# Optimization experiments

Hardware: AMD Instinct MI355X
Metric: run time of the kernel (lower is better)

## Reference

```python
import jax, jax.numpy as jnp
import numpy as np

DIM = 256
NUM_HEADS = 4
HEAD_DIM = DIM // NUM_HEADS
SCALE = HEAD_DIM ** -0.5


def setup_inputs() -> dict:
    key = jax.random.key(0)
    ks = jax.random.split(key, 11)
    B, Nq, Nkv = 4, 2048, 2048
    inp = {
        "query_feat": jax.random.normal(ks[0], (B, Nq, DIM), dtype=jnp.float32),
        "key_value_feat": jax.random.normal(ks[1], (B, Nkv, DIM), dtype=jnp.float32),
        "reliability_kv": jax.random.uniform(ks[2], (B, Nkv), dtype=jnp.float32),
        "Wq": jax.random.normal(ks[3], (DIM, DIM), dtype=jnp.float32) * (DIM ** -0.5),
        "bq": jnp.zeros((DIM,), jnp.float32),
        "Wk": jax.random.normal(ks[4], (DIM, DIM), dtype=jnp.float32) * (DIM ** -0.5),
        "bk": jnp.zeros((DIM,), jnp.float32),
        "Wv": jax.random.normal(ks[5], (DIM, DIM), dtype=jnp.float32) * (DIM ** -0.5),
        "bv": jnp.zeros((DIM,), jnp.float32),
        "Wo": jax.random.normal(ks[6], (DIM, DIM), dtype=jnp.float32) * (DIM ** -0.5),
        "bo": jnp.zeros((DIM,), jnp.float32),
    }
    return inp


def _heads(x):
    B, N, C = x.shape
    return x.reshape(B, N, NUM_HEADS, HEAD_DIM).transpose(0, 2, 1, 3)  # [B,H,N,hd]


def reference(query_feat, key_value_feat, reliability_kv, Wq, bq, Wk, bk, Wv, bv, Wo, bo):
    B, Nq, _ = query_feat.shape
    q = _heads(query_feat @ Wq + bq)          # [B,H,Nq,hd]
    k = _heads(key_value_feat @ Wk + bk)      # [B,H,Nkv,hd]
    v = _heads(key_value_feat @ Wv + bv)
    # gate K/V by reliability (broadcast over heads and head_dim)
    rk = reliability_kv[:, None, :, None]     # [B,1,Nkv,1]
    k = k * rk
    v = v * rk
    attn = jnp.einsum("bhqd,bhkd->bhqk", q, k) * SCALE
    log_r = jnp.log(jnp.clip(reliability_kv, 1e-6))[:, None, None, :]  # [B,1,1,Nkv]
    attn = jax.nn.softmax(attn + log_r, axis=-1)  # [B,H,Nq,Nkv]
    out = jnp.einsum("bhqk,bhkd->bhqd", attn, v)
    out = out.transpose(0, 2, 1, 3).reshape(B, Nq, DIM)
    out = out @ Wo + bo
    attn_mean = attn.mean(axis=1)  # [B,Nq,Nkv]
    return out, attn_mean
```

## Files before the change

kernel.cpp:

```cpp
#include <hip/hip_runtime.h>


typedef __attribute__((ext_vector_type(8))) _Float16 half8;
typedef __attribute__((ext_vector_type(4))) _Float16 half4;
typedef __attribute__((ext_vector_type(2))) __fp16 fp16x2;
typedef __attribute__((ext_vector_type(4))) float f32x4;

#define MFMAH32(A, B, C) __builtin_amdgcn_mfma_f32_16x16x32_f16((A), (B), (C), 0, 0, 0)
#define MFMAH16(A, B, C) __builtin_amdgcn_mfma_f32_16x16x16f16((A), (B), (C), 0, 0, 0)

__device__ __forceinline__ unsigned short f2h(float f) {
    union { _Float16 h; unsigned short u; } c; c.h = (_Float16)f; return c.u;
}
__device__ __forceinline__ float h2f(unsigned short u) {
    union { unsigned short u; _Float16 h; } c; c.u = u; return (float)c.h;
}
__device__ __forceinline__ half8 ldh8(const unsigned short* p) {
    return *reinterpret_cast<const half8*>(p);
}
__device__ __forceinline__ half4 ldh4(const unsigned short* p) {
    return *reinterpret_cast<const half4*>(p);
}
__device__ __forceinline__ half4 pk4(float a, float b, float c, float d) {
    union { fp16x2 h2[2]; half4 h4; } u;
    u.h2[0] = __builtin_amdgcn_cvt_pkrtz(a, b);
    u.h2[1] = __builtin_amdgcn_cvt_pkrtz(c, d);
    return u.h4;
}
__device__ __forceinline__ unsigned int pku(float a, float b) {
    union { fp16x2 h2; unsigned int u; } c;
    c.h2 = __builtin_amdgcn_cvt_pkrtz(a, b);
    return c.u;
}
__device__ __forceinline__ void gld16(const unsigned short* g, unsigned short* l) {
    __builtin_amdgcn_global_load_lds(
        (const __attribute__((address_space(1))) unsigned int*)g,
        (__attribute__((address_space(3))) unsigned int*)l, 16, 0, 0);
}

__global__ void wsplit_kernel(const float* __restrict__ Wq, const float* __restrict__ Wk,
                              const float* __restrict__ Wv, const float* __restrict__ Wo,
                              unsigned short* __restrict__ WT) {
    int e = blockIdx.x * 256 + threadIdx.x;
    int m = e >> 16;
    int idx = e & 65535;
    int k = idx >> 8, n = idx & 255;
    const float* W = (m == 0) ? Wq : (m == 1) ? Wk : (m == 2) ? Wv : Wo;
    WT[m * 65536 + n * 256 + k] = f2h(W[idx]);
}

#define STAGE_W(dst_, src_, kt_) do {                                               \
    _Pragma("unroll")                                                               \
    for (int j_ = 0; j_ < 4; ++j_) {                                                \
        int s_ = w * 4 + j_;                                                        \
        int rowl_ = 8 * s_ + (l >> 3);                                              \
        int so_ = rowl_ * 256 + (kt_) * 64 + (((l & 7) ^ (rowl_ & 7)) << 3);        \
        gld16(&(src_)[so_], &(dst_)[s_ * 512]);                                     \
    }                                                                               \
} while (0)

#define GEMM_TILE(buf_, kt_) do {                                                   \
    _Pragma("unroll")                                                               \
    for (int ksl_ = 0; ksl_ < 2; ++ksl_) {                                          \
        _Pragma("unroll")                                                           \
        for (int n_ = 0; n_ < 16; ++n_) {                                           \
            int r_ = n_ * 16 + l15;                                                 \
            int idx_ = r_ * 64 + ((((ksl_)*4 + lg) ^ (r_ & 7)) << 3);               \
            half8 b_ = ldh8(&(buf_)[idx_]);                                         \
            acc[n_] = MFMAH32(ah[(kt_) * 2 + ksl_], b_, acc[n_]);                   \
        }                                                                           \
    }                                                                               \
} while (0)

__global__ __launch_bounds__(512, 1) void proj3_kernel(
    const float* __restrict__ query, const float* __restrict__ kv,
    const float* __restrict__ rel, const unsigned short* __restrict__ WT,
    const float* __restrict__ bq, const float* __restrict__ bk, const float* __restrict__ bv,
    unsigned short* __restrict__ Qh, unsigned short* __restrict__ Kh,
    unsigned short* __restrict__ Vtmp) {
    const int job = blockIdx.y;
    const float* X = (job == 0) ? query : kv;
    const unsigned short* wg = WT + job * 65536;
    const float* bias = (job == 0) ? bq : (job == 1) ? bk : bv;
    const float* rs = (job == 0) ? nullptr : rel;
    unsigned short* oh = (job == 0) ? Qh : (job == 1) ? Kh : Vtmp;

    __shared__ __align__(16) unsigned short wlds[2][256 * 64];

    const int w = threadIdx.x >> 6, l = threadIdx.x & 63;
    const int l15 = l & 15, lg = l >> 4;
    const int arow = blockIdx.x * 128 + w * 16 + l15;

    half8 ah[8];
#pragma unroll
    for (int ks = 0; ks < 8; ++ks) {
        const float* p = &X[arow * 256 + ks * 32 + lg * 8];
        float4 f0 = *reinterpret_cast<const float4*>(p);
        float4 f1 = *reinterpret_cast<const float4*>(p + 4);
        half8 t;
        t[0] = (_Float16)f0.x; t[1] = (_Float16)f0.y; t[2] = (_Float16)f0.z; t[3] = (_Float16)f0.w;
        t[4] = (_Float16)f1.x; t[5] = (_Float16)f1.y; t[6] = (_Float16)f1.z; t[7] = (_Float16)f1.w;
        ah[ks] = t;
    }
    f32x4 acc[16];
#pragma unroll
    for (int n = 0; n < 16; ++n) acc[n] = (f32x4){0.f, 0.f, 0.f, 0.f};

    STAGE_W(wlds[0], wg, 0);
    __syncthreads();
#pragma unroll
    for (int kt = 0; kt < 4; ++kt) {
        const int cur = kt & 1, nx = cur ^ 1;
        if (kt < 3) STAGE_W(wlds[nx], wg, kt + 1);
        GEMM_TILE(wlds[cur], kt);
        __syncthreads();
    }

    const int orow0 = blockIdx.x * 128 + w * 16 + lg * 4;
    float rsv[4];
#pragma unroll
    for (int r = 0; r < 4; ++r) rsv[r] = rs ? rs[orow0 + r] : 1.0f;
#pragma unroll
    for (int n = 0; n < 16; ++n) {
        const int col = n * 16 + l15;
        const float bn = bias[col];
#pragma unroll
        for (int r = 0; r < 4; ++r)
            oh[(orow0 + r) * 256 + col] = f2h((acc[n][r] + bn) * rsv[r]);
    }
}

__global__ void transpose_v_kernel(const unsigned short* __restrict__ Vtmp,
                                   unsigned short* __restrict__ Vt) {
    __shared__ unsigned short tile[16][264];
    const int st = blockIdx.x, b = blockIdx.y;
    const int t = threadIdx.x;
#pragma unroll
    for (int it = 0; it < 4; ++it) {
        int idx = it * 256 + t;
        int kr = idx >> 6;
        int d4 = (idx & 63) * 4;
        ushort4 v = *reinterpret_cast<const ushort4*>(
            &Vtmp[(size_t)(b * 2048 + st * 16 + kr) * 256 + d4]);
        tile[kr][d4 + 0] = v.x; tile[kr][d4 + 1] = v.y;
        tile[kr][d4 + 2] = v.z; tile[kr][d4 + 3] = v.w;
    }
    __syncthreads();
    {
        const int d = t;
        unsigned int u[8];
#pragma unroll
        for (int k2 = 0; k2 < 8; ++k2)
            u[k2] = (unsigned int)tile[k2 * 2][d] | ((unsigned int)tile[k2 * 2 + 1][d] << 16);
        uint4* dst = reinterpret_cast<uint4*>(&Vt[((size_t)(b * 128 + st) * 256 + d) * 16]);
        dst[0] = (uint4){u[0], u[1], u[2], u[3]};
        dst[1] = (uint4){u[4], u[5], u[6], u[7]};
    }
}

__global__ __launch_bounds__(512, 4) void attn_pass1(
    const unsigned short* __restrict__ Qh, const unsigned short* __restrict__ Kh,
    const unsigned short* __restrict__ Vt, const float* __restrict__ rel,
    float* __restrict__ po_a, float* __restrict__ po_b, float* __restrict__ ps) {
    const int bid = blockIdx.x;
    const int sw = (bid & 7) * 64 + (bid >> 3);
    const int b = sw >> 7;
    const int rem = sw & 127;
    const int kh = rem & 1;
    const int q0 = (rem >> 1) * 32;
    const int tid = threadIdx.x;
    const int w = tid >> 6, h = w & 3, ks = w >> 2;
    const int l = tid & 63, l15 = l & 15, lg = l >> 4;
    const float C2 = 0.18033688011112042f;

    __shared__ __align__(16) unsigned short ldsK[8][2][1024];
    __shared__ __align__(16) unsigned short ldsV[8][2][1024];
    __shared__ float rel_lr[2048];
    __shared__ float ssum_sh[2][4][2][16];

    {
        float4 v = reinterpret_cast<const float4*>(&rel[b * 2048])[tid];
        float* d = &rel_lr[tid * 4];
        d[0] = log2f(fmaxf(v.x, 1e-6f)); d[1] = log2f(fmaxf(v.y, 1e-6f));
        d[2] = log2f(fmaxf(v.z, 1e-6f)); d[3] = log2f(fmaxf(v.w, 1e-6f));
    }

    half8 qf00, qf01, qf10, qf11;
    {
        const int o0 = (b * 2048 + q0 + l15) * 256 + h * 64 + lg * 8;
        const int o1 = o0 + 16 * 256;
        qf00 = ldh8(&Qh[o0]); qf01 = ldh8(&Qh[o0 + 32]);
        qf10 = ldh8(&Qh[o1]); qf11 = ldh8(&Qh[o1 + 32]);
    }
    __syncthreads();

    const int st0 = kh * 64 + ks * 32;

#define STG(buf_, i_) do {                                                          \
    const unsigned short* kbp_ = Kh + (size_t)(b * 2048 + (st0 + (i_)) * 16) * 256  \
                                 + h * 64;                                          \
    _Pragma("unroll")                                                               \
    for (int j_ = 0; j_ < 2; ++j_) {                                                \
        int r_ = j_ * 8 + (l >> 3);                                                 \
        gld16(kbp_ + r_ * 256 + (((l & 7) ^ ((l >> 3) & 7)) << 3),                  \
              &ldsK[w][buf_][j_ * 512]);                                            \
    }                                                                               \
    const unsigned short* vbp_ = Vt + (size_t)((b * 128 + st0 + (i_)) * 256         \
                                 + h * 64) * 16;                                    \
    _Pragma("unroll")                                                               \
    for (int j_ = 0; j_ < 2; ++j_) {                                                \
        int d_ = j_ * 32 + (l >> 1);                                                \
        gld16(vbp_ + d_ * 16 + (((l & 1) ^ ((l >> 1) & 1)) << 3),                   \
              &ldsV[w][buf_][j_ * 512]);                                            \
    }                                                                               \
} while (0)

    float ssum0 = 0.f, ssum1 = 0.f;
    f32x4 o0acc[4], o1acc[4];
#pragma unroll
    for (int dc = 0; dc < 4; ++dc) {
        o0acc[dc] = (f32x4){0.f, 0.f, 0.f, 0.f};
        o1acc[dc] = (f32x4){0.f, 0.f, 0.f, 0.f};
    }

    STG(0, 0);
    for (int i = 0; i < 32; ++i) {
        const int cur = i & 1, nx = cur ^ 1;
        if (i < 31) {
            STG(nx, i + 1);
            asm volatile("s_waitcnt vmcnt(4)" ::: "memory");
        } else {
            asm volatile("s_waitcnt vmcnt(0)" ::: "memory");
        }
        __builtin_amdgcn_sched_barrier(0);
        half8 kf0 = ldh8(&ldsK[w][cur][l15 * 64 + ((lg ^ (l15 & 7)) << 3)]);
        half8 kf1 = ldh8(&ldsK[w][cur][l15 * 64 + (((4 + lg) ^ (l15 & 7)) << 3)]);
        f32x4 a0 = (f32x4){0.f, 0.f, 0.f, 0.f}, a1 = a0;
        a0 = MFMAH32(kf0, qf00, a0); a0 = MFMAH32(kf1, qf01, a0);
        a1 = MFMAH32(kf0, qf10, a1); a1 = MFMAH32(kf1, qf11, a1);
        float4 lr4 = *reinterpret_cast<const float4*>(&rel_lr[(st0 + i) * 16 + lg * 4]);
        float p00 = exp2f(__builtin_fmaf(a0[0], C2, lr4.x));
        float p01 = exp2f(__builtin_fmaf(a0[1], C2, lr4.y));
        float p02 = exp2f(__builtin_fmaf(a0[2], C2, lr4.z));
        float p03 = exp2f(__builtin_fmaf(a0[3], C2, lr4.w));
        float p10 = exp2f(__builtin_fmaf(a1[0], C2, lr4.x));
        float p11 = exp2f(__builtin_fmaf(a1[1], C2, lr4.y));
        float p12 = exp2f(__builtin_fmaf(a1[2], C2, lr4.z));
        float p13 = exp2f(__builtin_fmaf(a1[3], C2, lr4.w));
        ssum0 += (p00 + p01) + (p02 + p03);
        ssum1 += (p10 + p11) + (p12 + p13);
        half4 pa0 = pk4(p00, p01, p02, p03);
        half4 pa1 = pk4(p10, p11, p12, p13);
#pragma unroll
        for (int dc = 0; dc < 4; ++dc) {
            const int d = dc * 16 + l15;
            half4 vf = ldh4(&ldsV[w][cur][d * 16 + ((((lg >> 1) ^ (d & 1))) << 3) + (lg & 1) * 4]);
            o0acc[dc] = MFMAH16(pa0, vf, o0acc[dc]);
            o1acc[dc] = MFMAH16(pa1, vf, o1acc[dc]);
        }
    }
#undef STG

    float v0 = ssum0, v1 = ssum1;
    v0 += __shfl_xor(v0, 16); v0 += __shfl_xor(v0, 32);
    v1 += __shfl_xor(v1, 16); v1 += __shfl_xor(v1, 32);

    __syncthreads();
    if (l < 16) { ssum_sh[ks][h][0][l] = v0; ssum_sh[ks][h][1][l] = v1; }
    float* obuf = (float*)&ldsK[0][0][0];
    if (ks == 1) {
#pragma unroll
        for (int dc = 0; dc < 4; ++dc)
#pragma unroll
            for (int r = 0; r < 4; ++r) {
                const int d = h * 64 + dc * 16 + l15;
                obuf[(lg * 4 + r) * 256 + d] = o0acc[dc][r];
                obuf[(16 + lg * 4 + r) * 256 + d] = o1acc[dc][r];
            }
    }
    __syncthreads();
    if (ks == 0) {
        const int chunk = b * 2 + kh;
        float* po = (chunk < 2) ? (po_a + (size_t)chunk * 524288)
                                : (po_b + (size_t)(chunk - 2) * 524288);
#pragma unroll
        for (int dc = 0; dc < 4; ++dc)
#pragma unroll
            for (int r = 0; r < 4; ++r) {
                const int d = h * 64 + dc * 16 + l15;
                const int qa = lg * 4 + r, qb = 16 + lg * 4 + r;
                po[(size_t)(q0 + qa) * 256 + d] = o0acc[dc][r] + obuf[qa * 256 + d];
                po[(size_t)(q0 + qb) * 256 + d] = o1acc[dc][r] + obuf[qb * 256 + d];
            }
        if (l < 16) {
            ps[(chunk * 4 + h) * 2048 + q0 + l] =
                ssum_sh[0][h][0][l] + ssum_sh[1][h][0][l];
            ps[(chunk * 4 + h) * 2048 + q0 + 16 + l] =
                ssum_sh[0][h][1][l] + ssum_sh[1][h][1][l];
        }
    }
}

__global__ __launch_bounds__(256) void combine_kernel(
    const float* __restrict__ po_a, const float* __restrict__ po_b,
    const float* __restrict__ ps, unsigned short* __restrict__ AO,
    float* __restrict__ sinv_ws) {
    const int t = blockIdx.x * 256 + threadIdx.x;
    const int d4 = t & 63;
    const int bq = t >> 6;
    const int q = bq & 2047;
    const int b = bq >> 11;
    const int d0 = d4 * 4, h = d0 >> 6;
    const int c0 = b * 2, c1 = b * 2 + 1;
    const float* p0 = (c0 < 2) ? po_a + (size_t)c0 * 524288 : po_b + (size_t)(c0 - 2) * 524288;
    const float* p1 = (c1 < 2) ? po_a + (size_t)c1 * 524288 : po_b + (size_t)(c1 - 2) * 524288;
    float4 x = *reinterpret_cast<const float4*>(&p0[(size_t)q * 256 + d0]);
    float4 y = *reinterpret_cast<const float4*>(&p1[(size_t)q * 256 + d0]);
    float s = ps[(c0 * 4 + h) * 2048 + q] + ps[(c1 * 4 + h) * 2048 + q];
    float si = 1.0f / s;
    ushort4 o;
    o.x = f2h((x.x + y.x) * si); o.y = f2h((x.y + y.y) * si);
    o.z = f2h((x.z + y.z) * si); o.w = f2h((x.w + y.w) * si);
    *reinterpret_cast<ushort4*>(&AO[((size_t)(b * 2048 + q)) * 256 + d0]) = o;
    if (d4 == (h << 4)) sinv_ws[(b * 4 + h) * 2048 + q] = si;
}

__global__ __launch_bounds__(256, 2) void attn_mean_kernel(
    const unsigned short* __restrict__ Qh, const unsigned short* __restrict__ Kh,
    const float* __restrict__ rel, const float* __restrict__ sinv_ws,
    float* __restrict__ attn_mean) {
    const int kslice = blockIdx.x >> 8;
    const int inner = blockIdx.x & 255;
    const int sw = (inner & 7) * 32 + (inner >> 3);
    const int b = sw >> 6;
    const int q0 = (sw & 63) * 32;
    const int tid = threadIdx.x;
    const int w = tid >> 6;
    const int h = w;
    const int l = tid & 63, l15 = l & 15, lg = l >> 4;
    const int kb = b * 2048;
    const float C2 = 0.18033688011112042f;

    __shared__ __align__(16) unsigned short ldsK[2][8192];
    __shared__ __align__(16) unsigned short pbf2[2][4][2][640];
    __shared__ float rel_lr[2048];

#define STAGE_KM(dst_, kt_) do {                                                    \
    _Pragma("unroll")                                                               \
    for (int j_ = 0; j_ < 4; ++j_) {                                                \
        int s_ = w * 4 + j_;                                                        \
        int r_ = 2 * s_ + (l >> 5);                                                 \
        size_t so_ = (size_t)(kb + (kt_) * 32 + r_) * 256 +                         \
                     (((l & 31) ^ (r_ & 7)) << 3);                                  \
        gld16(&Kh[so_], &(dst_)[s_ * 512]);                                         \
    }                                                                               \
} while (0)

    {
        float4 v0 = reinterpret_cast<const float4*>(&rel[b * 2048])[tid * 2];
        float4 v1 = reinterpret_cast<const float4*>(&rel[b * 2048])[tid * 2 + 1];
        float* d = &rel_lr[tid * 8];
        d[0] = log2f(fmaxf(v0.x, 1e-6f)); d[1] = log2f(fmaxf(v0.y, 1e-6f));
        d[2] = log2f(fmaxf(v0.z, 1e-6f)); d[3] = log2f(fmaxf(v0.w, 1e-6f));
        d[4] = log2f(fmaxf(v1.x, 1e-6f)); d[5] = log2f(fmaxf(v1.y, 1e-6f));
        d[6] = log2f(fmaxf(v1.z, 1e-6f)); d[7] = log2f(fmaxf(v1.w, 1e-6f));
    }

    half8 qf00, qf01, qf10, qf11;
    {
        const int o0 = (b * 2048 + q0 + l15) * 256 + h * 64 + lg * 8;
        const int o1 = o0 + 16 * 256;
        qf00 = ldh8(&Qh[o0]); qf01 = ldh8(&Qh[o0 + 32]);
        qf10 = ldh8(&Qh[o1]); qf11 = ldh8(&Qh[o1 + 32]);
    }
    const float lsi0 = log2f(sinv_ws[(b * 4 + h) * 2048 + q0 + l15]) - 2.0f;
    const float lsi1 = log2f(sinv_ws[(b * 4 + h) * 2048 + q0 + 16 + l15]) - 2.0f;
    __syncthreads();

    const int kt0 = kslice * 8;
    STAGE_KM(ldsK[0], kt0);
    for (int ki = 0; ki < 8; ++ki) {
        const int kt = kt0 + ki;
        const int cur = ki & 1, nx = cur ^ 1;
        if (ki < 7) {
            STAGE_KM(ldsK[nx], kt + 1);
            asm volatile("s_waitcnt vmcnt(4)" ::: "memory");
        } else {
            asm volatile("s_waitcnt vmcnt(0)" ::: "memory");
        }
        asm volatile("s_barrier" ::: "memory");
        __builtin_amdgcn_sched_barrier(0);
#pragma unroll
        for (int kc = 0; kc < 2; ++kc) {
            const int r = kc * 16 + l15;
            const int rx = r & 7;
            half8 kf0 = ldh8(&ldsK[cur][r * 256 + (((h * 8 + lg) ^ rx) << 3)]);
            half8 kf1 = ldh8(&ldsK[cur][r * 256 + (((h * 8 + 4 + lg) ^ rx) << 3)]);
            f32x4 a0 = (f32x4){0.f, 0.f, 0.f, 0.f}, a1 = a0;
            a0 = MFMAH32(kf0, qf00, a0); a0 = MFMAH32(kf1, qf01, a0);
            a1 = MFMAH32(kf0, qf10, a1); a1 = MFMAH32(kf1, qf11, a1);
            float4 lr4 = *reinterpret_cast<const float4*>(
                &rel_lr[kt * 32 + kc * 16 + lg * 4]);
            float q00 = exp2f(__builtin_fmaf(a0[0], C2, lsi0) + lr4.x);
            float q01 = exp2f(__builtin_fmaf(a0[1], C2, lsi0) + lr4.y);
            float q02 = exp2f(__builtin_fmaf(a0[2], C2, lsi0) + lr4.z);
            float q03 = exp2f(__builtin_fmaf(a0[3], C2, lsi0) + lr4.w);
            float q10 = exp2f(__builtin_fmaf(a1[0], C2, lsi1) + lr4.x);
            float q11 = exp2f(__builtin_fmaf(a1[1], C2, lsi1) + lr4.y);
            float q12 = exp2f(__builtin_fmaf(a1[2], C2, lsi1) + lr4.z);
            float q13 = exp2f(__builtin_fmaf(a1[3], C2, lsi1) + lr4.w);
            uint2 w0, w1;
            w0.x = pku(q00, q01); w0.y = pku(q02, q03);
            w1.x = pku(q10, q11); w1.y = pku(q12, q13);
            *reinterpret_cast<uint2*>(&pbf2[cur][h][0][l15 * 40 + kc * 16 + lg * 4]) = w0;
            *reinterpret_cast<uint2*>(&pbf2[cur][h][1][l15 * 40 + kc * 16 + lg * 4]) = w1;
        }
        asm volatile("s_waitcnt lgkmcnt(0)\n\ts_barrier" ::: "memory");
        {
            const int qs_ = tid >> 7, row = (tid >> 3) & 15, kq = tid & 7;
            float m0 = 0.f, m1 = 0.f, m2 = 0.f, m3 = 0.f;
#pragma unroll
            for (int hh = 0; hh < 4; ++hh) {
                ushort4 u = *reinterpret_cast<const ushort4*>(
                    &pbf2[cur][hh][qs_][row * 40 + kq * 4]);
                m0 += h2f(u.x); m1 += h2f(u.y); m2 += h2f(u.z); m3 += h2f(u.w);
            }
            *reinterpret_cast<float4*>(
                &attn_mean[(size_t)(b * 2048 + q0 + qs_ * 16 + row) * 2048 +
                           kt * 32 + kq * 4]) = (float4){m0, m1, m2, m3};
        }
    }
#undef STAGE_KM
}

__global__ __launch_bounds__(512, 1) void final_kernel(
    const unsigned short* __restrict__ AO, const unsigned short* __restrict__ WoT,
    const float* __restrict__ bo, float* __restrict__ out) {
    __shared__ __align__(16) unsigned short wlds[2][256 * 64];

    const int w = threadIdx.x >> 6, l = threadIdx.x & 63;
    const int l15 = l & 15, lg = l >> 4;
    const int arow = blockIdx.x * 128 + w * 16 + l15;

    half8 ah[8];
#pragma unroll
    for (int ks = 0; ks < 8; ++ks)
        ah[ks] = ldh8(&AO[arow * 256 + ks * 32 + lg * 8]);
    f32x4 acc[16];
#pragma unroll
    for (int n = 0; n < 16; ++n) acc[n] = (f32x4){0.f, 0.f, 0.f, 0.f};

    STAGE_W(wlds[0], WoT, 0);
    __syncthreads();
#pragma unroll
    for (int kt = 0; kt < 4; ++kt) {
        const int cur = kt & 1, nx = cur ^ 1;
        if (kt < 3) STAGE_W(wlds[nx], WoT, kt + 1);
        GEMM_TILE(wlds[cur], kt);
        __syncthreads();
    }

    const int orow0 = blockIdx.x * 128 + w * 16 + lg * 4;
#pragma unroll
    for (int n = 0; n < 16; ++n) {
        const int col = n * 16 + l15;
        const float bn = bo[col];
#pragma unroll
        for (int r = 0; r < 4; ++r)
            out[(orow0 + r) * 256 + col] = acc[n][r] + bn;
    }
}

extern "C" void kernel_launch(void* const* d_in, const int* in_sizes, int n_in,
                              void* d_out, int out_size, void* d_ws, size_t ws_size,
                              hipStream_t stream) {
    const float* query = (const float*)d_in[0];
    const float* kv    = (const float*)d_in[1];
    const float* rel   = (const float*)d_in[2];
    const float* Wq    = (const float*)d_in[3];
    const float* bq    = (const float*)d_in[4];
    const float* Wk    = (const float*)d_in[5];
    const float* bk    = (const float*)d_in[6];
    const float* Wv    = (const float*)d_in[7];
    const float* bv    = (const float*)d_in[8];
    const float* Wo    = (const float*)d_in[9];
    const float* bo    = (const float*)d_in[10];

    char* ws = (char*)d_ws;
    unsigned short* WT   = (unsigned short*)(ws + 0);
    unsigned short* Qh   = (unsigned short*)(ws + 524288);
    unsigned short* Kh   = (unsigned short*)(ws + 4718592);
    unsigned short* Vtmp = (unsigned short*)(ws + 8912896);
    unsigned short* Vt   = (unsigned short*)(ws + 13107200);
    unsigned short* AO   = (unsigned short*)(ws + 17301504);
    float*          sinv = (float*)(ws + 21495808);
    float*          ps   = (float*)(ws + 21626880);
    float*          po_b = (float*)(ws + 21889024);
    float*          po_a = (float*)Vtmp;

    float* out = (float*)d_out;
    float* attn_mean = (float*)d_out + 2097152;

    wsplit_kernel<<<1024, 256, 0, stream>>>(Wq, Wk, Wv, Wo, WT);
    proj3_kernel<<<dim3(64, 3), 512, 0, stream>>>(query, kv, rel, WT,
                                                  bq, bk, bv, Qh, Kh, Vtmp);
    transpose_v_kernel<<<dim3(128, 4), 256, 0, stream>>>(Vtmp, Vt);
    attn_pass1<<<512, 512, 0, stream>>>(Qh, Kh, Vt, rel, po_a, po_b, ps);
    combine_kernel<<<2048, 256, 0, stream>>>(po_a, po_b, ps, AO, sinv);
    attn_mean_kernel<<<2048, 256, 0, stream>>>(Qh, Kh, rel, sinv, attn_mean);
    final_kernel<<<64, 512, 0, stream>>>(AO, WT + 3 * 65536, bo, out);
}
```

Before: 123.1 us.

## Reduce attn_mean over heads in registers instead of through LDS

```diff
diff --git a/kernel.cpp b/kernel.cpp
--- a/kernel.cpp
+++ b/kernel.cpp
@@ -26,11 +26,6 @@
     u.h2[0] = __builtin_amdgcn_cvt_pkrtz(a, b);
     u.h2[1] = __builtin_amdgcn_cvt_pkrtz(c, d);
     return u.h4;
-}
-__device__ __forceinline__ unsigned int pku(float a, float b) {
-    union { fp16x2 h2; unsigned int u; } c;
-    c.h2 = __builtin_amdgcn_cvt_pkrtz(a, b);
-    return c.u;
 }
 __device__ __forceinline__ void gld16(const unsigned short* g, unsigned short* l) {
     __builtin_amdgcn_global_load_lds(
@@ -325,7 +320,7 @@
     if (d4 == (h << 4)) sinv_ws[(b * 4 + h) * 2048 + q] = si;
 }
 
-__global__ __launch_bounds__(256, 2) void attn_mean_kernel(
+__global__ __launch_bounds__(256, 4) void attn_mean_kernel(
     const unsigned short* __restrict__ Qh, const unsigned short* __restrict__ Kh,
     const float* __restrict__ rel, const float* __restrict__ sinv_ws,
     float* __restrict__ attn_mean) {
@@ -336,13 +331,12 @@
     const int q0 = (sw & 63) * 32;
     const int tid = threadIdx.x;
     const int w = tid >> 6;
-    const int h = w;
+    const int qs = w >> 1, kc = w & 1;
     const int l = tid & 63, l15 = l & 15, lg = l >> 4;
     const int kb = b * 2048;
     const float C2 = 0.18033688011112042f;
 
     __shared__ __align__(16) unsigned short ldsK[2][8192];
-    __shared__ __align__(16) unsigned short pbf2[2][4][2][640];
     __shared__ float rel_lr[2048];
 
 #define STAGE_KM(dst_, kt_) do {                                                    \
@@ -366,15 +360,21 @@
         d[6] = log2f(fmaxf(v1.z, 1e-6f)); d[7] = log2f(fmaxf(v1.w, 1e-6f));
     }
 
-    half8 qf00, qf01, qf10, qf11;
+    half8 qf[4][2];
     {
-        const int o0 = (b * 2048 + q0 + l15) * 256 + h * 64 + lg * 8;
-        const int o1 = o0 + 16 * 256;
-        qf00 = ldh8(&Qh[o0]); qf01 = ldh8(&Qh[o0 + 32]);
-        qf10 = ldh8(&Qh[o1]); qf11 = ldh8(&Qh[o1 + 32]);
-    }
-    const float lsi0 = log2f(sinv_ws[(b * 4 + h) * 2048 + q0 + l15]) - 2.0f;
-    const float lsi1 = log2f(sinv_ws[(b * 4 + h) * 2048 + q0 + 16 + l15]) - 2.0f;
+        const int qrow = b * 2048 + q0 + qs * 16 + l15;
+#pragma unroll
+        for (int h = 0; h < 4; ++h)
+#pragma unroll
+            for (int kd = 0; kd < 2; ++kd)
+                qf[h][kd] = ldh8(&Qh[qrow * 256 + h * 64 + kd * 32 + lg * 8]);
+    }
+    float lsi[4][4];
+#pragma unroll
+    for (int h = 0; h < 4; ++h)
+#pragma unroll
+        for (int r4 = 0; r4 < 4; ++r4)
+            lsi[h][r4] = log2f(sinv_ws[(b * 4 + h) * 2048 + q0 + qs * 16 + lg * 4 + r4]) - 2.0f;
     __syncthreads();
 
     const int kt0 = kslice * 8;
@@ -390,45 +390,29 @@
         }
         asm volatile("s_barrier" ::: "memory");
         __builtin_amdgcn_sched_barrier(0);
-#pragma unroll
-        for (int kc = 0; kc < 2; ++kc) {
-            const int r = kc * 16 + l15;
-            const int rx = r & 7;
+        const int r = kc * 16 + l15;
+        const int rx = r & 7;
+        f32x4 a[4];
+#pragma unroll
+        for (int h = 0; h < 4; ++h) {
             half8 kf0 = ldh8(&ldsK[cur][r * 256 + (((h * 8 + lg) ^ rx) << 3)]);
             half8 kf1 = ldh8(&ldsK[cur][r * 256 + (((h * 8 + 4 + lg) ^ rx) << 3)]);
-            f32x4 a0 = (f32x4){0.f, 0.f, 0.f, 0.f}, a1 = a0;
-            a0 = MFMAH32(kf0, qf00, a0); a0 = MFMAH32(kf1, qf01, a0);
-            a1 = MFMAH32(kf0, qf10, a1); a1 = MFMAH32(kf1, qf11, a1);
-            float4 lr4 = *reinterpret_cast<const float4*>(
-                &rel_lr[kt * 32 + kc * 16 + lg * 4]);
-            float q00 = exp2f(__builtin_fmaf(a0[0], C2, lsi0) + lr4.x);
-            float q01 = exp2f(__builtin_fmaf(a0[1], C2, lsi0) + lr4.y);
-            float q02 = exp2f(__builtin_fmaf(a0[2], C2, lsi0) + lr4.z);
-            float q03 = exp2f(__builtin_fmaf(a0[3], C2, lsi0) + lr4.w);
-            float q10 = exp2f(__builtin_fmaf(a1[0], C2, lsi1) + lr4.x);
-            float q11 = exp2f(__builtin_fmaf(a1[1], C2, lsi1) + lr4.y);
-            float q12 = exp2f(__builtin_fmaf(a1[2], C2, lsi1) + lr4.z);
-            float q13 = exp2f(__builtin_fmaf(a1[3], C2, lsi1) + lr4.w);
-            uint2 w0, w1;
-            w0.x = pku(q00, q01); w0.y = pku(q02, q03);
-            w1.x = pku(q10, q11); w1.y = pku(q12, q13);
-            *reinterpret_cast<uint2*>(&pbf2[cur][h][0][l15 * 40 + kc * 16 + lg * 4]) = w0;
-            *reinterpret_cast<uint2*>(&pbf2[cur][h][1][l15 * 40 + kc * 16 + lg * 4]) = w1;
+            f32x4 t = (f32x4){0.f, 0.f, 0.f, 0.f};
+            t = MFMAH32(qf[h][0], kf0, t);
+            t = MFMAH32(qf[h][1], kf1, t);
+            a[h] = t;
+        }
+        const float lr = rel_lr[kt * 32 + kc * 16 + l15];
+        const size_t kcol = (size_t)(kt * 32 + kc * 16 + l15);
+#pragma unroll
+        for (int r4 = 0; r4 < 4; ++r4) {
+            float m = exp2f(__builtin_fmaf(a[0][r4], C2, lsi[0][r4]) + lr)
+                    + exp2f(__builtin_fmaf(a[1][r4], C2, lsi[1][r4]) + lr)
+                    + exp2f(__builtin_fmaf(a[2][r4], C2, lsi[2][r4]) + lr)
+                    + exp2f(__builtin_fmaf(a[3][r4], C2, lsi[3][r4]) + lr);
+            attn_mean[(size_t)(b * 2048 + q0 + qs * 16 + lg * 4 + r4) * 2048 + kcol] = m;
         }
         asm volatile("s_waitcnt lgkmcnt(0)\n\ts_barrier" ::: "memory");
-        {
-            const int qs_ = tid >> 7, row = (tid >> 3) & 15, kq = tid & 7;
-            float m0 = 0.f, m1 = 0.f, m2 = 0.f, m3 = 0.f;
-#pragma unroll
-            for (int hh = 0; hh < 4; ++hh) {
-                ushort4 u = *reinterpret_cast<const ushort4*>(
-                    &pbf2[cur][hh][qs_][row * 40 + kq * 4]);
-                m0 += h2f(u.x); m1 += h2f(u.y); m2 += h2f(u.z); m3 += h2f(u.w);
-            }
-            *reinterpret_cast<float4*>(
-                &attn_mean[(size_t)(b * 2048 + q0 + qs_ * 16 + row) * 2048 +
-                           kt * 32 + kq * 4]) = (float4){m0, m1, m2, m3};
-        }
     }
 #undef STAGE_KM
 }
```

New measurement: 111.8 us. 1.1x faster.
